# Kernel optimization log

Measured on AMD Instinct MI355X. Metric: run time of the kernel, lower is better.

Reference implementation:

```python
import jax, jax.numpy as jnp
import numpy as np

NUM_ITER = 3
NUM_BINS = 10
MAX_DISP = 4
BIN_DISP = 0.5
CHANNELS = 32
MIN_FILTER_REG = 1e-05
SEARCH = 2 * MAX_DISP + 1
CORR_CH = SEARCH * SEARCH  # 81


def local_cost_volume(f1, f2, d):
    """uflow-style local cost volume: mean over channels of f1 * shifted f2.
    f1, f2: (B,H,W,C) -> (B,H,W,(2d+1)^2)."""
    B, H, W, C = f1.shape
    f2p = jnp.pad(f2, ((0, 0), (d, d), (d, d), (0, 0)))
    s = 2 * d + 1
    cols = [jnp.mean(f1 * f2p[:, i:i + H, j:j + W, :], axis=-1)
            for i in range(s) for j in range(s)]
    return jnp.stack(cols, axis=-1)


def compute_distance_map():
    # (1, SEARCH, SEARCH, NUM_BINS) soft-binned displacement distances
    bins = jnp.arange(NUM_BINS, dtype=jnp.float32).reshape(1, 1, 1, NUM_BINS)
    disp = jnp.arange(-MAX_DISP, MAX_DISP + 1, dtype=jnp.float32)
    k0 = disp.reshape(1, SEARCH, 1, 1)
    k1 = disp.reshape(1, 1, SEARCH, 1)
    dist = jnp.sqrt(k0 * k0 + k1 * k1)
    bin_diff = dist / BIN_DISP - bins
    # faithful to source: slice along axis=1 (spatial rows), as written in TF code
    bin_val = jnp.concatenate(
        [jax.nn.relu(1.0 - jnp.abs(bin_diff[:, :-1, :, :])),
         jnp.clip(1.0 + bin_diff[:, -1:, :, :], 0.0, 1.0)], axis=1)
    return bin_val


def leaky_par(x, a):
    return (1.0 - a) / 2.0 * jnp.abs(x) + (1.0 + a) / 2.0 * x


def leaky_par_deriv(x, a):
    return (1.0 - a) / 2.0 * jnp.sign(jax.lax.stop_gradient(x)) + (1.0 + a) / 2.0


def setup_inputs() -> dict:
    key = jax.random.key(0)
    ks = jax.random.split(key, 4)
    B, H, W, C = 4, 256, 256, CHANNELS
    d = jnp.arange(NUM_BINS, dtype=jnp.float32) * BIN_DISP
    gauss = jnp.exp(-0.5 * d * d)  # init_gauss_sigma = 1.0
    return {
        "reference_feature": jax.random.normal(ks[0], (B, H, W, C), jnp.float32),
        "query_feature": jax.random.normal(ks[1], (B, H, W, C), jnp.float32),
        "beta": jnp.ones((1,), jnp.float32),
        "target_map_w": gauss - jnp.min(gauss),                 # (NUM_BINS,)
        "spatial_w": jnp.ones((NUM_BINS,), jnp.float32),        # (NUM_BINS,)
        "mask_w": 4.0 * jnp.tanh(2.0 - d),                      # (NUM_BINS,)
        "mr_w": jax.random.normal(ks[2], (CORR_CH, CHANNELS), jnp.float32) * 0.05,
        "mr_b": jnp.zeros((CHANNELS,), jnp.float32),
        "lr_w": jax.random.normal(ks[3], (CORR_CH, CHANNELS), jnp.float32) * 0.05,
        "lr_b": jnp.zeros((CHANNELS,), jnp.float32),
        "w_reg": 0.01 * jnp.ones((1,), jnp.float32),
        "log_step_length": jnp.zeros((1,), jnp.float32),
    }


def reference(reference_feature, query_feature, beta, target_map_w, spatial_w,
              mask_w, mr_w, mr_b, lr_w, lr_b, w_reg, log_step_length):
    C = reference_feature.shape[-1]
    # filter initializer: beta * feat / (mean(feat^2) + eps)
    w = beta * reference_feature / (
        jnp.mean(reference_feature * reference_feature, axis=-1, keepdims=True) + 1e-06)
    reg_weight = jnp.clip(w_reg * w_reg, MIN_FILTER_REG ** 2 / C ** 2, None)
    step_length = jnp.exp(log_step_length)

    dm = compute_distance_map()                     # (1,9,9,NUM_BINS)
    y = jnp.einsum('ahwb,b->ahw', dm, target_map_w).reshape(1, 1, 1, -1)       # (1,1,1,81)
    v_plus = jnp.einsum('ahwb,b->ahw', dm, spatial_w).reshape(1, 1, 1, -1)     # (1,1,1,81)
    weight_m = jax.nn.sigmoid(jnp.einsum('ahwb,b->ahw', dm, mask_w)).reshape(1, 1, 1, -1)

    for _ in range(NUM_ITER):
        c = local_cost_volume(w, reference_feature, MAX_DISP)        # (B,H,W,81)
        act = v_plus * leaky_par(c, weight_m)
        dact = v_plus * leaky_par_deriv(c, weight_m)
        res = act - v_plus * y
        mapped = jnp.einsum('bhwk,kc->bhwc', dact * res, mr_w) + mr_b  # 81 -> 32
        fg_loss = jnp.einsum('bhwk,kc->bhwc',
                             local_cost_volume(mapped, reference_feature, MAX_DISP),
                             lr_w) + lr_b                              # 81 -> 32
        filter_grad = reg_weight * w + fg_loss
        scores = dact * local_cost_volume(filter_grad, reference_feature, MAX_DISP)
        alpha_den = jnp.sum(scores * scores, axis=-1, keepdims=True)
        alpha_num = jnp.sum(filter_grad * filter_grad, axis=-1, keepdims=True)
        alpha = alpha_num / alpha_den
        w = w + alpha * step_length * filter_grad
    return w
```

## Files before the change

### kernel.cpp

```cpp
#include <hip/hip_runtime.h>

#define B_ 4
#define H_ 256
#define W_ 256
#define PXF4 9

__device__ __forceinline__ float dot32f(const float* a, const float4* r) {
    float s0 = 0.f, s1 = 0.f, s2 = 0.f, s3 = 0.f;
#pragma unroll
    for (int u = 0; u < 8; ++u) {
        float4 q = r[u];
        s0 += a[4*u+0] * q.x; s1 += a[4*u+1] * q.y;
        s2 += a[4*u+2] * q.z; s3 += a[4*u+3] * q.w;
    }
    return (s0 + s1) + (s2 + s3);
}

template<int TSX, int TSY, int NTH>
__global__ void __launch_bounds__(NTH)
gocor(const float* __restrict__ rf_g,
      const float* __restrict__ beta_p, const float* __restrict__ tw_p,
      const float* __restrict__ sw_p,  const float* __restrict__ mw_p,
      const float* __restrict__ mrw_p, const float* __restrict__ mrb_p,
      const float* __restrict__ lrw_p, const float* __restrict__ lrb_p,
      const float* __restrict__ wreg_p, const float* __restrict__ lsl_p,
      float* __restrict__ out)
{
    constexpr int TWXc = TSX + 8, TWYc = TSY + 8, NPXc = TWXc * TWYc;
    extern __shared__ float4 smem[];
    float4* s_rf  = smem;
    float4* s_kp  = smem + NPXc * PXF4;
    float*  s_bias = (float*)(s_kp + 81);

    const int tid = threadIdx.x;
    const int tx = tid % TSX, ty = tid / TSX;
    const int bx = blockIdx.x * TSX, by = blockIdx.y * TSY, bb = blockIdx.z;
    const float* rfb = rf_g + (size_t)bb * H_ * W_ * 32;

    for (int idx = tid; idx < NPXc * 8; idx += NTH) {
        int u = idx & 7, p = idx >> 3;
        int ly = p / TWXc, lx = p - ly * TWXc;
        int gy = by + ly - 4, gx = bx + lx - 4;
        float4 v = make_float4(0.f, 0.f, 0.f, 0.f);
        if (gy >= 0 && gy < H_ && gx >= 0 && gx < W_)
            v = *(const float4*)(rfb + ((size_t)(gy * W_ + gx)) * 32 + u * 4);
        s_rf[p * PXF4 + u] = v;
    }

    if (tid < 81) {
        int i = tid / 9, j = tid % 9;
        float di = (float)(i - 4), dj = (float)(j - 4);
        float dist = sqrtf(di * di + dj * dj);
        float y = 0.f, vp = 0.f, m = 0.f;
        for (int b = 0; b < 10; ++b) {
            float bd = 2.f * dist - (float)b;
            float val;
            if (i < 8) val = fmaxf(0.f, 1.f - fabsf(bd));
            else       val = fminf(1.f, fmaxf(0.f, 1.f + bd));
            y  += val * tw_p[b];
            vp += val * sw_p[b];
            m  += val * mw_p[b];
        }
        float wm = 1.f / (1.f + expf(-m));
        s_kp[tid] = make_float4(vp * 0.5f * (1.f - wm),
                                vp * 0.5f * (1.f + wm),
                                vp * y, 0.f);
    }
    if (tid < 32)      s_bias[tid]      = mrb_p[tid];
    else if (tid < 64) s_bias[tid]      = lrb_p[tid - 32];

    float beta = beta_p[0];
    float wr   = wreg_p[0];
    float regw = fmaxf(wr * wr, (1e-5f * 1e-5f) / (32.f * 32.f));
    float step = expf(lsl_p[0]);

    __syncthreads();

    float w[32];
    {
        const float4* r = &s_rf[(((ty + 4) * TWXc) + (tx + 4)) * PXF4];
#pragma unroll
        for (int u = 0; u < 8; ++u) {
            float4 q = r[u];
            w[4*u+0] = q.x; w[4*u+1] = q.y; w[4*u+2] = q.z; w[4*u+3] = q.w;
        }
        float msq = 0.f;
#pragma unroll
        for (int c = 0; c < 32; ++c) msq += w[c] * w[c];
        float inv = beta / (msq * (1.f / 32.f) + 1e-6f);
#pragma unroll
        for (int c = 0; c < 32; ++c) w[c] *= inv;
    }

    float mp[32], fg[32];

    for (int it = 0; it < 3; ++it) {
        unsigned long long sp0 = 0ull, sn0 = 0ull;
        unsigned int sp1 = 0u, sn1 = 0u;
#pragma unroll
        for (int c = 0; c < 32; ++c) mp[c] = s_bias[c];
        for (int i = 0; i < 9; ++i) {
            int rowbase = (ty + i) * TWXc + tx;
            for (int j = 0; j < 9; ++j) {
                int k = i * 9 + j;
                const float4* r = &s_rf[(rowbase + j) * PXF4];
                float ck = dot32f(w, r) * (1.f / 32.f);
                if (ck > 0.f)      { if (k < 64) sp0 |= 1ull << k; else sp1 |= 1u << (k - 64); }
                else if (ck < 0.f) { if (k < 64) sn0 |= 1ull << k; else sn1 |= 1u << (k - 64); }
                float4 kp = s_kp[k];
                float sg = (ck > 0.f) ? 1.f : ((ck < 0.f) ? -1.f : 0.f);
                float act  = kp.x * fabsf(ck) + kp.y * ck;
                float res  = act - kp.z;
                float dact = kp.x * sg + kp.y;
                float s = dact * res;
                const float* mr = mrw_p + k * 32;
#pragma unroll
                for (int c = 0; c < 32; ++c) mp[c] += s * mr[c];
            }
        }

#pragma unroll
        for (int c = 0; c < 32; ++c) fg[c] = s_bias[32 + c] + regw * w[c];
        for (int i = 0; i < 9; ++i) {
            int rowbase = (ty + i) * TWXc + tx;
            for (int j = 0; j < 9; ++j) {
                int k = i * 9 + j;
                const float4* r = &s_rf[(rowbase + j) * PXF4];
                float ck = dot32f(mp, r) * (1.f / 32.f);
                const float* lr = lrw_p + k * 32;
#pragma unroll
                for (int c = 0; c < 32; ++c) fg[c] += ck * lr[c];
            }
        }

        float num = 0.f;
#pragma unroll
        for (int c = 0; c < 32; ++c) num += fg[c] * fg[c];
        float den = 0.f;
        for (int i = 0; i < 9; ++i) {
            int rowbase = (ty + i) * TWXc + tx;
            for (int j = 0; j < 9; ++j) {
                int k = i * 9 + j;
                const float4* r = &s_rf[(rowbase + j) * PXF4];
                float c3 = dot32f(fg, r) * (1.f / 32.f);
                bool bp = (k < 64) ? ((sp0 >> k) & 1ull) : ((sp1 >> (k - 64)) & 1u);
                bool bn = (k < 64) ? ((sn0 >> k) & 1ull) : ((sn1 >> (k - 64)) & 1u);
                float sg = bp ? 1.f : (bn ? -1.f : 0.f);
                float4 kp = s_kp[k];
                float dact = kp.x * sg + kp.y;
                float s3 = dact * c3;
                den += s3 * s3;
            }
        }
        float as = (num / den) * step;
#pragma unroll
        for (int c = 0; c < 32; ++c) w[c] += as * fg[c];
    }

    float* o = out + (((size_t)bb * H_ + (by + ty)) * W_ + (bx + tx)) * 32;
#pragma unroll
    for (int u = 0; u < 8; ++u)
        *(float4*)(o + u * 4) = make_float4(w[4*u+0], w[4*u+1], w[4*u+2], w[4*u+3]);
}

static const size_t BIG_SHM   = (size_t)(40 * 24 * PXF4 + 81 + 16) * 16;
static const size_t SMALL_SHM = (size_t)(24 * 16 * PXF4 + 81 + 16) * 16;

static bool query_big_path() {
    int dev = 0;
    if (hipGetDevice(&dev) != hipSuccess) return false;
    hipFuncSetAttribute(reinterpret_cast<const void*>(&gocor<32, 16, 512>),
                        hipFuncAttributeMaxDynamicSharedMemorySize, (int)BIG_SHM);
    int maxShm = 0;
    if (hipDeviceGetAttribute(&maxShm, hipDeviceAttributeMaxSharedMemoryPerBlock, dev) == hipSuccess &&
        (size_t)maxShm >= BIG_SHM)
        return true;
    hipFuncAttributes fa;
    if (hipFuncGetAttributes(&fa, reinterpret_cast<const void*>(&gocor<32, 16, 512>)) == hipSuccess &&
        (size_t)fa.maxDynamicSharedSizeBytes >= BIG_SHM)
        return true;
    return false;
}

extern "C" void kernel_launch(void* const* d_in, const int* in_sizes, int n_in,
                              void* d_out, int out_size, void* d_ws, size_t ws_size,
                              hipStream_t stream) {
    (void)d_ws; (void)ws_size; (void)in_sizes; (void)n_in; (void)out_size;
    static const bool use_big = query_big_path();

    const float* rf   = (const float*)d_in[0];
    const float* beta = (const float*)d_in[2];
    const float* tw   = (const float*)d_in[3];
    const float* sw   = (const float*)d_in[4];
    const float* mw   = (const float*)d_in[5];
    const float* mrw  = (const float*)d_in[6];
    const float* mrb  = (const float*)d_in[7];
    const float* lrw  = (const float*)d_in[8];
    const float* lrb  = (const float*)d_in[9];
    const float* wreg = (const float*)d_in[10];
    const float* lsl  = (const float*)d_in[11];
    float* o = (float*)d_out;

    if (use_big) {
        dim3 grid(W_ / 32, H_ / 16, B_);
        hipLaunchKernelGGL((gocor<32, 16, 512>), grid, dim3(512), BIG_SHM, stream,
                           rf, beta, tw, sw, mw, mrw, mrb, lrw, lrb, wreg, lsl, o);
    } else {
        dim3 grid(W_ / 16, H_ / 8, B_);
        hipLaunchKernelGGL((gocor<16, 8, 128>), grid, dim3(128), SMALL_SHM, stream,
                           rf, beta, tw, sw, mw, mrw, mrb, lrw, lrb, wreg, lsl, o);
    }
}
```

Measured before the change: 677.5 us.

## Process two vertically adjacent pixels per thread to reuse shared-memory reference loads

Adds a new kernel where each thread computes two pixels in adjacent rows, so each loaded reference feature vector in the 10-row sweep serves both pixels' cost-volume entries. The block shrinks from 512 to 256 threads over the same 32x16 tile with launch bounds of one block per wave slot. Loads are software-pipelined with double-buffered float4 registers. This targets LDS bandwidth and per-tap load overhead, at the cost of roughly doubled register state (w, mp, fg for two pixels) and possible spills or lower occupancy.

```diff
diff --git a/kernel.cpp b/kernel.cpp
--- a/kernel.cpp
+++ b/kernel.cpp
@@ -14,6 +14,220 @@
         s2 += a[4*u+2] * q.z; s3 += a[4*u+3] * q.w;
     }
     return (s0 + s1) + (s2 + s3);
+}
+
+__device__ __forceinline__ float dot32q(const float* a, const float4* q) {
+    float s0 = 0.f, s1 = 0.f, s2 = 0.f, s3 = 0.f;
+#pragma unroll
+    for (int u = 0; u < 8; ++u) {
+        float4 v = q[u];
+        s0 += a[4*u+0] * v.x; s1 += a[4*u+1] * v.y;
+        s2 += a[4*u+2] * v.z; s3 += a[4*u+3] * v.w;
+    }
+    return (s0 + s1) + (s2 + s3);
+}
+
+template<int TSX, int TSYH, int NTH>
+__global__ void __launch_bounds__(NTH, 1)
+gocor2(const float* __restrict__ rf_g,
+       const float* __restrict__ beta_p, const float* __restrict__ tw_p,
+       const float* __restrict__ sw_p,  const float* __restrict__ mw_p,
+       const float* __restrict__ mrw_p, const float* __restrict__ mrb_p,
+       const float* __restrict__ lrw_p, const float* __restrict__ lrb_p,
+       const float* __restrict__ wreg_p, const float* __restrict__ lsl_p,
+       float* __restrict__ out)
+{
+    constexpr int TWXc = TSX + 8, TWYc = 2*TSYH + 8, NPXc = TWXc * TWYc;
+    extern __shared__ float4 smem[];
+    float4* s_rf  = smem;
+    float4* s_kp  = smem + NPXc * PXF4;
+    float*  s_bias = (float*)(s_kp + 81);
+
+    const int tid = threadIdx.x;
+    const int tx = tid % TSX, ty = tid / TSX;
+    const int ty2 = 2 * ty;
+    const int bx = blockIdx.x * TSX, by = blockIdx.y * (2*TSYH), bb = blockIdx.z;
+    const float* rfb = rf_g + (size_t)bb * H_ * W_ * 32;
+
+    for (int idx = tid; idx < NPXc * 8; idx += NTH) {
+        int u = idx & 7, p = idx >> 3;
+        int ly = p / TWXc, lx = p - ly * TWXc;
+        int gy = by + ly - 4, gx = bx + lx - 4;
+        float4 v = make_float4(0.f, 0.f, 0.f, 0.f);
+        if (gy >= 0 && gy < H_ && gx >= 0 && gx < W_)
+            v = *(const float4*)(rfb + ((size_t)(gy * W_ + gx)) * 32 + u * 4);
+        s_rf[p * PXF4 + u] = v;
+    }
+
+    if (tid < 81) {
+        int i = tid / 9, j = tid % 9;
+        float di = (float)(i - 4), dj = (float)(j - 4);
+        float dist = sqrtf(di * di + dj * dj);
+        float y = 0.f, vp = 0.f, m = 0.f;
+        for (int b = 0; b < 10; ++b) {
+            float bd = 2.f * dist - (float)b;
+            float val;
+            if (i < 8) val = fmaxf(0.f, 1.f - fabsf(bd));
+            else       val = fminf(1.f, fmaxf(0.f, 1.f + bd));
+            y  += val * tw_p[b];
+            vp += val * sw_p[b];
+            m  += val * mw_p[b];
+        }
+        float wm = 1.f / (1.f + expf(-m));
+        s_kp[tid] = make_float4(vp * 0.5f * (1.f - wm),
+                                vp * 0.5f * (1.f + wm),
+                                vp * y, 0.f);
+    }
+    if (tid < 32)      s_bias[tid] = mrb_p[tid];
+    else if (tid < 64) s_bias[tid] = lrb_p[tid - 32];
+
+    float beta = beta_p[0];
+    float wr   = wreg_p[0];
+    float regw = fmaxf(wr * wr, (1e-5f * 1e-5f) / (32.f * 32.f));
+    float step = expf(lsl_p[0]);
+
+    __syncthreads();
+
+    float w0[32], w1[32];
+    {
+        const float4* r0 = &s_rf[(((ty2 + 4) * TWXc) + (tx + 4)) * PXF4];
+        const float4* r1 = &s_rf[(((ty2 + 5) * TWXc) + (tx + 4)) * PXF4];
+#pragma unroll
+        for (int u = 0; u < 8; ++u) {
+            float4 q0 = r0[u], q1 = r1[u];
+            w0[4*u+0] = q0.x; w0[4*u+1] = q0.y; w0[4*u+2] = q0.z; w0[4*u+3] = q0.w;
+            w1[4*u+0] = q1.x; w1[4*u+1] = q1.y; w1[4*u+2] = q1.z; w1[4*u+3] = q1.w;
+        }
+        float m0 = 0.f, m1 = 0.f;
+#pragma unroll
+        for (int c = 0; c < 32; ++c) { m0 += w0[c] * w0[c]; m1 += w1[c] * w1[c]; }
+        float i0 = beta / (m0 * (1.f / 32.f) + 1e-6f);
+        float i1 = beta / (m1 * (1.f / 32.f) + 1e-6f);
+#pragma unroll
+        for (int c = 0; c < 32; ++c) { w0[c] *= i0; w1[c] *= i1; }
+    }
+
+    float mp0[32], mp1[32], fg0[32], fg1[32];
+
+#define LOADQ(Q, JJ) do { const float4* _r = &s_rf[(rowbase + (JJ)) * PXF4]; \
+    _Pragma("unroll") for (int _u = 0; _u < 8; ++_u) (Q)[_u] = _r[_u]; } while (0)
+
+    for (int it = 0; it < 3; ++it) {
+        unsigned long long spa0 = 0ull, sna0 = 0ull, spb0 = 0ull, snb0 = 0ull;
+        unsigned int spa1 = 0u, sna1 = 0u, spb1 = 0u, snb1 = 0u;
+
+        auto bodyA = [&](int k, const float4* q, const float* w, float* mp,
+                         unsigned long long& sp0, unsigned long long& sn0,
+                         unsigned int& sp1, unsigned int& sn1) {
+            float ck = dot32q(w, q) * (1.f / 32.f);
+            if (ck > 0.f)      { if (k < 64) sp0 |= 1ull << k; else sp1 |= 1u << (k - 64); }
+            else if (ck < 0.f) { if (k < 64) sn0 |= 1ull << k; else sn1 |= 1u << (k - 64); }
+            float4 kp = s_kp[k];
+            float sg = (ck > 0.f) ? 1.f : ((ck < 0.f) ? -1.f : 0.f);
+            float act  = kp.x * fabsf(ck) + kp.y * ck;
+            float res  = act - kp.z;
+            float dact = kp.x * sg + kp.y;
+            float s = dact * res;
+            const float* mr = mrw_p + k * 32;
+#pragma unroll
+            for (int c = 0; c < 32; ++c) mp[c] += s * mr[c];
+        };
+#pragma unroll
+        for (int c = 0; c < 32; ++c) { mp0[c] = s_bias[c]; mp1[c] = s_bias[c]; }
+#pragma unroll 1
+        for (int dy = 0; dy < 10; ++dy) {
+            const int rowbase = (ty2 + dy) * TWXc + tx;
+            float4 qa[8], qb[8];
+            LOADQ(qa, 0);
+#pragma unroll 1
+            for (int j = 0; j < 8; j += 2) {
+                LOADQ(qb, j + 1);
+                if (dy < 9) bodyA(dy*9 + j,       qa, w0, mp0, spa0, sna0, spa1, sna1);
+                if (dy > 0) bodyA((dy-1)*9 + j,   qa, w1, mp1, spb0, snb0, spb1, snb1);
+                LOADQ(qa, j + 2);
+                if (dy < 9) bodyA(dy*9 + j+1,     qb, w0, mp0, spa0, sna0, spa1, sna1);
+                if (dy > 0) bodyA((dy-1)*9 + j+1, qb, w1, mp1, spb0, snb0, spb1, snb1);
+            }
+            if (dy < 9) bodyA(dy*9 + 8,       qa, w0, mp0, spa0, sna0, spa1, sna1);
+            if (dy > 0) bodyA((dy-1)*9 + 8,   qa, w1, mp1, spb0, snb0, spb1, snb1);
+        }
+
+        auto bodyB = [&](int k, const float4* q, const float* mp, float* fg) {
+            float ck = dot32q(mp, q) * (1.f / 32.f);
+            const float* lr = lrw_p + k * 32;
+#pragma unroll
+            for (int c = 0; c < 32; ++c) fg[c] += ck * lr[c];
+        };
+#pragma unroll
+        for (int c = 0; c < 32; ++c) {
+            fg0[c] = s_bias[32 + c] + regw * w0[c];
+            fg1[c] = s_bias[32 + c] + regw * w1[c];
+        }
+#pragma unroll 1
+        for (int dy = 0; dy < 10; ++dy) {
+            const int rowbase = (ty2 + dy) * TWXc + tx;
+            float4 qa[8], qb[8];
+            LOADQ(qa, 0);
+#pragma unroll 1
+            for (int j = 0; j < 8; j += 2) {
+                LOADQ(qb, j + 1);
+                if (dy < 9) bodyB(dy*9 + j,       qa, mp0, fg0);
+                if (dy > 0) bodyB((dy-1)*9 + j,   qa, mp1, fg1);
+                LOADQ(qa, j + 2);
+                if (dy < 9) bodyB(dy*9 + j+1,     qb, mp0, fg0);
+                if (dy > 0) bodyB((dy-1)*9 + j+1, qb, mp1, fg1);
+            }
+            if (dy < 9) bodyB(dy*9 + 8,       qa, mp0, fg0);
+            if (dy > 0) bodyB((dy-1)*9 + 8,   qa, mp1, fg1);
+        }
+
+        auto bodyC = [&](int k, const float4* q, const float* fg,
+                         unsigned long long sp0, unsigned long long sn0,
+                         unsigned int sp1, unsigned int sn1, float& den) {
+            float c3 = dot32q(fg, q) * (1.f / 32.f);
+            bool bp = (k < 64) ? (((sp0 >> k) & 1ull) != 0) : (((sp1 >> (k - 64)) & 1u) != 0);
+            bool bn = (k < 64) ? (((sn0 >> k) & 1ull) != 0) : (((sn1 >> (k - 64)) & 1u) != 0);
+            float sg = bp ? 1.f : (bn ? -1.f : 0.f);
+            float4 kp = s_kp[k];
+            float dact = kp.x * sg + kp.y;
+            float s3 = dact * c3;
+            den += s3 * s3;
+        };
+        float num0 = 0.f, num1 = 0.f;
+#pragma unroll
+        for (int c = 0; c < 32; ++c) { num0 += fg0[c] * fg0[c]; num1 += fg1[c] * fg1[c]; }
+        float den0 = 0.f, den1 = 0.f;
+#pragma unroll 1
+        for (int dy = 0; dy < 10; ++dy) {
+            const int rowbase = (ty2 + dy) * TWXc + tx;
+            float4 qa[8], qb[8];
+            LOADQ(qa, 0);
+#pragma unroll 1
+            for (int j = 0; j < 8; j += 2) {
+                LOADQ(qb, j + 1);
+                if (dy < 9) bodyC(dy*9 + j,       qa, fg0, spa0, sna0, spa1, sna1, den0);
+                if (dy > 0) bodyC((dy-1)*9 + j,   qa, fg1, spb0, snb0, spb1, snb1, den1);
+                LOADQ(qa, j + 2);
+                if (dy < 9) bodyC(dy*9 + j+1,     qb, fg0, spa0, sna0, spa1, sna1, den0);
+                if (dy > 0) bodyC((dy-1)*9 + j+1, qb, fg1, spb0, snb0, spb1, snb1, den1);
+            }
+            if (dy < 9) bodyC(dy*9 + 8,       qa, fg0, spa0, sna0, spa1, sna1, den0);
+            if (dy > 0) bodyC((dy-1)*9 + 8,   qa, fg1, spb0, snb0, spb1, snb1, den1);
+        }
+        float as0 = (num0 / den0) * step;
+        float as1 = (num1 / den1) * step;
+#pragma unroll
+        for (int c = 0; c < 32; ++c) { w0[c] += as0 * fg0[c]; w1[c] += as1 * fg1[c]; }
+    }
+#undef LOADQ
+
+    float* o0 = out + (((size_t)bb * H_ + (by + ty2)) * W_ + (bx + tx)) * 32;
+    float* o1 = o0 + (size_t)W_ * 32;
+#pragma unroll
+    for (int u = 0; u < 8; ++u) {
+        *(float4*)(o0 + u * 4) = make_float4(w0[4*u+0], w0[4*u+1], w0[4*u+2], w0[4*u+3]);
+        *(float4*)(o1 + u * 4) = make_float4(w1[4*u+0], w1[4*u+1], w1[4*u+2], w1[4*u+3]);
+    }
 }
 
 template<int TSX, int TSY, int NTH>
@@ -169,14 +383,14 @@
 static bool query_big_path() {
     int dev = 0;
     if (hipGetDevice(&dev) != hipSuccess) return false;
-    hipFuncSetAttribute(reinterpret_cast<const void*>(&gocor<32, 16, 512>),
+    hipFuncSetAttribute(reinterpret_cast<const void*>(&gocor2<32, 8, 256>),
                         hipFuncAttributeMaxDynamicSharedMemorySize, (int)BIG_SHM);
     int maxShm = 0;
     if (hipDeviceGetAttribute(&maxShm, hipDeviceAttributeMaxSharedMemoryPerBlock, dev) == hipSuccess &&
         (size_t)maxShm >= BIG_SHM)
         return true;
     hipFuncAttributes fa;
-    if (hipFuncGetAttributes(&fa, reinterpret_cast<const void*>(&gocor<32, 16, 512>)) == hipSuccess &&
+    if (hipFuncGetAttributes(&fa, reinterpret_cast<const void*>(&gocor2<32, 8, 256>)) == hipSuccess &&
         (size_t)fa.maxDynamicSharedSizeBytes >= BIG_SHM)
         return true;
     return false;
@@ -203,7 +417,7 @@
 
     if (use_big) {
         dim3 grid(W_ / 32, H_ / 16, B_);
-        hipLaunchKernelGGL((gocor<32, 16, 512>), grid, dim3(512), BIG_SHM, stream,
+        hipLaunchKernelGGL((gocor2<32, 8, 256>), grid, dim3(256), BIG_SHM, stream,
                            rf, beta, tw, sw, mw, mrw, mrb, lrw, lrb, wreg, lsl, o);
     } else {
         dim3 grid(W_ / 16, H_ / 8, B_);
```

Result: slower. 990.8 us (+46.2%).
